# Kernel tuning notes

Hardware: AMD Instinct MI355X
Metric: run time of the kernel (lower is better)

## Reference

```python
import jax, jax.numpy as jnp
import numpy as np

D_MODEL = 1024
HEADS = 16
DEPTH = D_MODEL // HEADS
B, S = 2, 2048


def setup_inputs() -> dict:
    key = jax.random.key(0)
    ks = jax.random.split(key, 12)
    s = 1.0 / np.sqrt(D_MODEL)
    return {
        "q": jax.random.normal(ks[0], (B, S, D_MODEL), jnp.float32),
        "k": jax.random.normal(ks[1], (B, S, D_MODEL), jnp.float32),
        "v": jax.random.normal(ks[2], (B, S, D_MODEL), jnp.float32),
        "mask": jnp.zeros((B, 1, 1, S), jnp.float32),
        "wq": jax.random.normal(ks[3], (D_MODEL, D_MODEL), jnp.float32) * s,
        "bq": jnp.zeros((D_MODEL,), jnp.float32),
        "wk": jax.random.normal(ks[4], (D_MODEL, D_MODEL), jnp.float32) * s,
        "bk": jnp.zeros((D_MODEL,), jnp.float32),
        "wv": jax.random.normal(ks[5], (D_MODEL, D_MODEL), jnp.float32) * s,
        "bv": jnp.zeros((D_MODEL,), jnp.float32),
        "wo": jax.random.normal(ks[6], (D_MODEL, D_MODEL), jnp.float32) * s,
        "bo": jnp.zeros((D_MODEL,), jnp.float32),
    }


def _split_heads(x):
    b, s, _ = x.shape
    return x.reshape(b, s, HEADS, DEPTH).transpose(0, 2, 1, 3)  # [B,H,S,D]


def reference(q, k, v, mask, wq, bq, wk, bk, wv, bv, wo, bo):
    qh = _split_heads(q @ wq + bq)
    kh = _split_heads(k @ wk + bk)
    vh = _split_heads(v @ wv + bv)
    scale = 1.0 / jnp.sqrt(jnp.asarray(DEPTH, jnp.float32))
    scores = jnp.einsum("bhqd,bhkd->bhqk", qh, kh) * scale
    scores = scores + mask * -1e9
    attn = jax.nn.softmax(scores, axis=-1)  # [B,H,Sq,Sk]
    ctx = jnp.einsum("bhqk,bhkd->bhqd", attn, vh)
    ctx = ctx.transpose(0, 2, 1, 3).reshape(q.shape[0], -1, D_MODEL)
    out = ctx @ wo + bo
    return out, attn
```

## Files before the change

kernel.cpp:

```cpp
#include <hip/hip_runtime.h>
#include <cstdint>
#include <cstddef>

#define DEV __device__ __forceinline__

typedef __attribute__((ext_vector_type(8))) __bf16 bf16x8;
typedef __attribute__((ext_vector_type(4))) float f32x4;
typedef __attribute__((ext_vector_type(4))) uint32_t u32x4;

constexpr int BB = 2, SS = 2048, DMOD = 1024, HH = 16, DDEP = 64;
constexpr int MM = BB * SS;
constexpr float SCL = 0.125f;

constexpr size_t SZ_ACT = (size_t)MM * DMOD * 2;
constexpr size_t SZ_W = (size_t)DMOD * DMOD * 2;
constexpr size_t OFF_QB = 0;
constexpr size_t OFF_KB = OFF_QB + SZ_ACT;
constexpr size_t OFF_VB = OFF_KB + SZ_ACT;
constexpr size_t OFF_WQT = OFF_VB + SZ_ACT;
constexpr size_t OFF_WKT = OFF_WQT + SZ_W;
constexpr size_t OFF_WVT = OFF_WKT + SZ_W;
constexpr size_t OFF_WOT = OFF_WVT + SZ_W;
constexpr size_t OFF_QH = OFF_WOT + SZ_W;
constexpr size_t OFF_KH = OFF_QH + SZ_ACT;
constexpr size_t OFF_VH = OFF_KH + SZ_ACT;
constexpr size_t OFF_VHT = OFF_QB;
constexpr size_t OFF_CTX = OFF_KB;

DEV uint16_t f2bf(float f) {
  uint32_t u = __builtin_bit_cast(uint32_t, f);
  u += 0x7fffu + ((u >> 16) & 1u);
  return (uint16_t)(u >> 16);
}
DEV uint32_t pk2(float a, float b) { return (uint32_t)f2bf(a) | ((uint32_t)f2bf(b) << 16); }
DEV f32x4 mfma16(bf16x8 a, bf16x8 b, f32x4 c) {
  return __builtin_amdgcn_mfma_f32_16x16x32_bf16(a, b, c, 0, 0, 0);
}

__global__ __launch_bounds__(256) void cast_bf16(const float4* __restrict__ in, u32x4* __restrict__ out) {
  size_t i = (size_t)blockIdx.x * 256 + threadIdx.x;
  float4 a = in[i * 2], b = in[i * 2 + 1];
  u32x4 o;
  o.x = pk2(a.x, a.y); o.y = pk2(a.z, a.w);
  o.z = pk2(b.x, b.y); o.w = pk2(b.z, b.w);
  out[i] = o;
}

__global__ __launch_bounds__(256) void wtrans(const float* __restrict__ W, uint16_t* __restrict__ WT) {
  __shared__ uint16_t tile[64 * 72];
  const int kb = blockIdx.x * 64, nb = blockIdx.y * 64;
  const int t = threadIdx.x;
  {
    const int kl = t >> 2, nc = (t & 3) * 16;
    const float4* src = reinterpret_cast<const float4*>(&W[(size_t)(kb + kl) * DMOD + nb + nc]);
    float4 v0 = src[0], v1 = src[1], v2 = src[2], v3 = src[3];
    uint16_t* d = &tile[kl * 72 + nc];
    d[0] = f2bf(v0.x); d[1] = f2bf(v0.y); d[2] = f2bf(v0.z); d[3] = f2bf(v0.w);
    d[4] = f2bf(v1.x); d[5] = f2bf(v1.y); d[6] = f2bf(v1.z); d[7] = f2bf(v1.w);
    d[8] = f2bf(v2.x); d[9] = f2bf(v2.y); d[10] = f2bf(v2.z); d[11] = f2bf(v2.w);
    d[12] = f2bf(v3.x); d[13] = f2bf(v3.y); d[14] = f2bf(v3.z); d[15] = f2bf(v3.w);
  }
  __syncthreads();
  {
    const int n = t >> 2, kc = (t & 3) * 16;
    uint16_t r[16];
#pragma unroll
    for (int j = 0; j < 16; ++j) r[j] = tile[(kc + j) * 72 + n];
    u32x4 o0, o1;
    o0.x = r[0] | ((uint32_t)r[1] << 16);  o0.y = r[2] | ((uint32_t)r[3] << 16);
    o0.z = r[4] | ((uint32_t)r[5] << 16);  o0.w = r[6] | ((uint32_t)r[7] << 16);
    o1.x = r[8] | ((uint32_t)r[9] << 16);  o1.y = r[10] | ((uint32_t)r[11] << 16);
    o1.z = r[12] | ((uint32_t)r[13] << 16); o1.w = r[14] | ((uint32_t)r[15] << 16);
    uint16_t* dst = &WT[(size_t)(nb + n) * DMOD + kb + kc];
    *reinterpret_cast<u32x4*>(dst) = o0;
    *reinterpret_cast<u32x4*>(dst + 8) = o1;
  }
}

__global__ __launch_bounds__(256) void vtrans(const uint16_t* __restrict__ Vh, uint16_t* __restrict__ VhT) {
  __shared__ uint16_t tile[64 * 72];
  const int sb = blockIdx.x * 64;
  const int bh = blockIdx.y;
  const int b = bh >> 4, h = bh & 15;
  const int t = threadIdx.x;
  {
    const int sl = t >> 2, dc = (t & 3) * 16;
    const u32x4* src = reinterpret_cast<const u32x4*>(&Vh[(size_t)(b * SS + sb + sl) * DMOD + h * DDEP + dc]);
    *reinterpret_cast<u32x4*>(&tile[sl * 72 + dc]) = src[0];
    *reinterpret_cast<u32x4*>(&tile[sl * 72 + dc + 8]) = src[1];
  }
  __syncthreads();
  {
    const int d = t >> 2, sc = (t & 3) * 16;
    uint16_t r[16];
#pragma unroll
    for (int j = 0; j < 16; ++j) r[j] = tile[(sc + j) * 72 + d];
    u32x4 o0, o1;
    o0.x = r[0] | ((uint32_t)r[1] << 16);  o0.y = r[2] | ((uint32_t)r[3] << 16);
    o0.z = r[4] | ((uint32_t)r[5] << 16);  o0.w = r[6] | ((uint32_t)r[7] << 16);
    o1.x = r[8] | ((uint32_t)r[9] << 16);  o1.y = r[10] | ((uint32_t)r[11] << 16);
    o1.z = r[12] | ((uint32_t)r[13] << 16); o1.w = r[14] | ((uint32_t)r[15] << 16);
    uint16_t* dst = &VhT[((size_t)bh * DDEP + d) * SS + sb + sc];
    *reinterpret_cast<u32x4*>(dst) = o0;
    *reinterpret_cast<u32x4*>(dst + 8) = o1;
  }
}

template <int OUTF32>
__global__ __launch_bounds__(256) void gemm_bt(
    const uint16_t* __restrict__ A, const uint16_t* __restrict__ Bt,
    const float* __restrict__ bias, void* __restrict__ Cout,
    int Md, int Nd, int Kd) {
  __shared__ uint16_t As[128 * 64];
  __shared__ uint16_t Bs[128 * 64];
  const int t = threadIdx.x;
  const int lane = t & 63, w = t >> 6;
  const int wr = w >> 1, wc = w & 1;
  const int g = lane >> 4, r16 = lane & 15;
  const int ntiles = Nd >> 7;
  const int mt = blockIdx.x / ntiles, nt = blockIdx.x % ntiles;
  char* AsB = reinterpret_cast<char*>(As);
  char* BsB = reinterpret_cast<char*>(Bs);

  f32x4 acc[4][4] = {};
  const int nkt = Kd >> 6;
  for (int kt = 0; kt < nkt; ++kt) {
#pragma unroll
    for (int i = 0; i < 4; ++i) {
      int idx = i * 256 + t;
      int row = idx >> 3, ch = idx & 7;
      int sw = row * 128 + ((ch * 16) ^ ((row & 7) << 4));
      *reinterpret_cast<u32x4*>(AsB + sw) =
          *reinterpret_cast<const u32x4*>(A + (size_t)(mt * 128 + row) * Kd + kt * 64 + ch * 8);
      *reinterpret_cast<u32x4*>(BsB + sw) =
          *reinterpret_cast<const u32x4*>(Bt + (size_t)(nt * 128 + row) * Kd + kt * 64 + ch * 8);
    }
    __syncthreads();
#pragma unroll
    for (int kk = 0; kk < 2; ++kk) {
      bf16x8 af[4], bfr[4];
#pragma unroll
      for (int mf = 0; mf < 4; ++mf) {
        int row = wr * 64 + mf * 16 + r16;
        af[mf] = *reinterpret_cast<const bf16x8*>(AsB + row * 128 + ((kk * 64 + g * 16) ^ ((row & 7) << 4)));
      }
#pragma unroll
      for (int nf = 0; nf < 4; ++nf) {
        int row = wc * 64 + nf * 16 + r16;
        bfr[nf] = *reinterpret_cast<const bf16x8*>(BsB + row * 128 + ((kk * 64 + g * 16) ^ ((row & 7) << 4)));
      }
#pragma unroll
      for (int mf = 0; mf < 4; ++mf)
#pragma unroll
        for (int nf = 0; nf < 4; ++nf)
          acc[mf][nf] = mfma16(af[mf], bfr[nf], acc[mf][nf]);
    }
    __syncthreads();
  }
  float bv[4];
#pragma unroll
  for (int nf = 0; nf < 4; ++nf) bv[nf] = bias[nt * 128 + wc * 64 + nf * 16 + r16];
#pragma unroll
  for (int mf = 0; mf < 4; ++mf)
#pragma unroll
    for (int nf = 0; nf < 4; ++nf)
#pragma unroll
      for (int r = 0; r < 4; ++r) {
        int row = mt * 128 + wr * 64 + mf * 16 + g * 4 + r;
        int col = nt * 128 + wc * 64 + nf * 16 + r16;
        float v0 = acc[mf][nf][r] + bv[nf];
        if (OUTF32)
          reinterpret_cast<float*>(Cout)[(size_t)row * Nd + col] = v0;
        else
          reinterpret_cast<uint16_t*>(Cout)[(size_t)row * Nd + col] = f2bf(v0);
      }
}

__global__ __launch_bounds__(256) void attn_fused(
    const uint16_t* __restrict__ Qh, const uint16_t* __restrict__ Kh,
    const uint16_t* __restrict__ VhT, const float* __restrict__ mask,
    float* __restrict__ attn, uint16_t* __restrict__ ctx) {
  __shared__ uint16_t Plds[4 * 32 * 128];
  const int t = threadIdx.x;
  const int lane = t & 63, w = t >> 6;
  const int g = lane >> 4, c16 = lane & 15;
  const int bid = blockIdx.x;
  const int bh = bid >> 4, qt = bid & 15;
  const int b = bh >> 4, h = bh & 15;

  const uint16_t* Qbase = Qh + ((size_t)(b * SS + qt * 128 + w * 32)) * DMOD + h * DDEP;
  const uint16_t* Kbase = Kh + ((size_t)b * SS) * DMOD + h * DDEP;
  const uint16_t* Vbase = VhT + (size_t)bh * DDEP * SS;
  const float* mbase = mask + (size_t)b * SS;
  char* Pw = reinterpret_cast<char*>(Plds) + w * (32 * 256);

  bf16x8 qf[2][2];
#pragma unroll
  for (int rf = 0; rf < 2; ++rf)
#pragma unroll
    for (int kk = 0; kk < 2; ++kk)
      qf[rf][kk] = *reinterpret_cast<const bf16x8*>(Qbase + (size_t)(rf * 16 + c16) * DMOD + kk * 32 + g * 8);

  float m_[2][4], l_[2][4];
#pragma unroll
  for (int rf = 0; rf < 2; ++rf)
#pragma unroll
    for (int r = 0; r < 4; ++r) { m_[rf][r] = -3.0e38f; l_[rf][r] = 0.f; }

  for (int kt = 0; kt < 16; ++kt) {
    f32x4 sacc[2][8] = {};
#pragma unroll
    for (int nf = 0; nf < 8; ++nf) {
      const uint16_t* kp = Kbase + (size_t)(kt * 128 + nf * 16 + c16) * DMOD + g * 8;
      bf16x8 b0 = *reinterpret_cast<const bf16x8*>(kp);
      bf16x8 b1 = *reinterpret_cast<const bf16x8*>(kp + 32);
      sacc[0][nf] = mfma16(qf[0][0], b0, sacc[0][nf]);
      sacc[0][nf] = mfma16(qf[0][1], b1, sacc[0][nf]);
      sacc[1][nf] = mfma16(qf[1][0], b0, sacc[1][nf]);
      sacc[1][nf] = mfma16(qf[1][1], b1, sacc[1][nf]);
    }
    float mv[8];
#pragma unroll
    for (int nf = 0; nf < 8; ++nf) mv[nf] = mbase[kt * 128 + nf * 16 + c16] * -1e9f;
#pragma unroll
    for (int rf = 0; rf < 2; ++rf) {
#pragma unroll
      for (int r = 0; r < 4; ++r) {
        float tm = -3.0e38f;
#pragma unroll
        for (int nf = 0; nf < 8; ++nf) {
          float sv = sacc[rf][nf][r] * SCL + mv[nf];
          sacc[rf][nf][r] = sv;
          tm = fmaxf(tm, sv);
        }
#pragma unroll
        for (int d = 1; d < 16; d <<= 1) tm = fmaxf(tm, __shfl_xor(tm, d));
        float mo = m_[rf][r];
        float mn = fmaxf(mo, tm);
        float sum = 0.f;
#pragma unroll
        for (int nf = 0; nf < 8; ++nf) sum += __expf(sacc[rf][nf][r] - mn);
#pragma unroll
        for (int d = 1; d < 16; d <<= 1) sum += __shfl_xor(sum, d);
        l_[rf][r] = l_[rf][r] * __expf(mo - mn) + sum;
        m_[rf][r] = mn;
      }
    }
  }
  float li[2][4];
#pragma unroll
  for (int rf = 0; rf < 2; ++rf)
#pragma unroll
    for (int r = 0; r < 4; ++r) li[rf][r] = 1.f / l_[rf][r];

  f32x4 cacc[2][4] = {};
  float* abase = attn + ((size_t)bh * SS + qt * 128 + w * 32) * SS;

  for (int kt = 0; kt < 16; ++kt) {
    f32x4 sacc[2][8] = {};
#pragma unroll
    for (int nf = 0; nf < 8; ++nf) {
      const uint16_t* kp = Kbase + (size_t)(kt * 128 + nf * 16 + c16) * DMOD + g * 8;
      bf16x8 b0 = *reinterpret_cast<const bf16x8*>(kp);
      bf16x8 b1 = *reinterpret_cast<const bf16x8*>(kp + 32);
      sacc[0][nf] = mfma16(qf[0][0], b0, sacc[0][nf]);
      sacc[0][nf] = mfma16(qf[0][1], b1, sacc[0][nf]);
      sacc[1][nf] = mfma16(qf[1][0], b0, sacc[1][nf]);
      sacc[1][nf] = mfma16(qf[1][1], b1, sacc[1][nf]);
    }
    float mv[8];
#pragma unroll
    for (int nf = 0; nf < 8; ++nf) mv[nf] = mbase[kt * 128 + nf * 16 + c16] * -1e9f;
#pragma unroll
    for (int rf = 0; rf < 2; ++rf)
#pragma unroll
      for (int nf = 0; nf < 8; ++nf)
#pragma unroll
        for (int r = 0; r < 4; ++r) {
          int prow = rf * 16 + g * 4 + r;
          float p = __expf(sacc[rf][nf][r] * SCL + mv[nf] - m_[rf][r]) * li[rf][r];
          abase[(size_t)prow * SS + kt * 128 + nf * 16 + c16] = p;
          *reinterpret_cast<uint16_t*>(
              Pw + prow * 256 + (((nf * 16 + c16) * 2) ^ ((prow & 7) << 4))) = f2bf(p);
        }
#pragma unroll
    for (int kk = 0; kk < 4; ++kk) {
      bf16x8 pa[2];
#pragma unroll
      for (int rf = 0; rf < 2; ++rf) {
        int arow = rf * 16 + c16;
        pa[rf] = *reinterpret_cast<const bf16x8*>(
            Pw + arow * 256 + ((kk * 64 + g * 16) ^ ((arow & 7) << 4)));
      }
#pragma unroll
      for (int nf = 0; nf < 4; ++nf) {
        bf16x8 vf = *reinterpret_cast<const bf16x8*>(
            Vbase + (size_t)(nf * 16 + c16) * SS + kt * 128 + kk * 32 + g * 8);
        cacc[0][nf] = mfma16(pa[0], vf, cacc[0][nf]);
        cacc[1][nf] = mfma16(pa[1], vf, cacc[1][nf]);
      }
    }
  }
#pragma unroll
  for (int rf = 0; rf < 2; ++rf)
#pragma unroll
    for (int nf = 0; nf < 4; ++nf)
#pragma unroll
      for (int r = 0; r < 4; ++r) {
        int row = qt * 128 + w * 32 + rf * 16 + g * 4 + r;
        ctx[((size_t)(b * SS + row)) * DMOD + h * DDEP + nf * 16 + c16] = f2bf(cacc[rf][nf][r]);
      }
}

extern "C" void kernel_launch(void* const* d_in, const int* in_sizes, int n_in,
                              void* d_out, int out_size, void* d_ws, size_t ws_size,
                              hipStream_t stream) {
  (void)in_sizes; (void)n_in; (void)out_size; (void)ws_size;
  const float* q = (const float*)d_in[0];
  const float* k = (const float*)d_in[1];
  const float* v = (const float*)d_in[2];
  const float* mask = (const float*)d_in[3];
  const float* wq = (const float*)d_in[4];
  const float* bq = (const float*)d_in[5];
  const float* wk = (const float*)d_in[6];
  const float* bk = (const float*)d_in[7];
  const float* wv = (const float*)d_in[8];
  const float* bvv = (const float*)d_in[9];
  const float* wo = (const float*)d_in[10];
  const float* bo = (const float*)d_in[11];

  char* ws = (char*)d_ws;
  uint16_t* qb = (uint16_t*)(ws + OFF_QB);
  uint16_t* kb = (uint16_t*)(ws + OFF_KB);
  uint16_t* vb = (uint16_t*)(ws + OFF_VB);
  uint16_t* wqT = (uint16_t*)(ws + OFF_WQT);
  uint16_t* wkT = (uint16_t*)(ws + OFF_WKT);
  uint16_t* wvT = (uint16_t*)(ws + OFF_WVT);
  uint16_t* woT = (uint16_t*)(ws + OFF_WOT);
  uint16_t* Qhp = (uint16_t*)(ws + OFF_QH);
  uint16_t* Khp = (uint16_t*)(ws + OFF_KH);
  uint16_t* Vhp = (uint16_t*)(ws + OFF_VH);
  uint16_t* VhTp = (uint16_t*)(ws + OFF_VHT);
  uint16_t* ctxp = (uint16_t*)(ws + OFF_CTX);

  float* outp = (float*)d_out;
  float* attnp = outp + (size_t)MM * DMOD;

  cast_bf16<<<2048, 256, 0, stream>>>((const float4*)q, (u32x4*)qb);
  cast_bf16<<<2048, 256, 0, stream>>>((const float4*)k, (u32x4*)kb);
  cast_bf16<<<2048, 256, 0, stream>>>((const float4*)v, (u32x4*)vb);
  wtrans<<<dim3(16, 16), 256, 0, stream>>>(wq, wqT);
  wtrans<<<dim3(16, 16), 256, 0, stream>>>(wk, wkT);
  wtrans<<<dim3(16, 16), 256, 0, stream>>>(wv, wvT);
  wtrans<<<dim3(16, 16), 256, 0, stream>>>(wo, woT);
  gemm_bt<0><<<256, 256, 0, stream>>>(qb, wqT, bq, Qhp, MM, DMOD, DMOD);
  gemm_bt<0><<<256, 256, 0, stream>>>(kb, wkT, bk, Khp, MM, DMOD, DMOD);
  gemm_bt<0><<<256, 256, 0, stream>>>(vb, wvT, bvv, Vhp, MM, DMOD, DMOD);
  vtrans<<<dim3(32, 32), 256, 0, stream>>>(Vhp, VhTp);
  attn_fused<<<512, 256, 0, stream>>>(Qhp, Khp, VhTp, mask, attnp, ctxp);
  gemm_bt<1><<<256, 256, 0, stream>>>(ctxp, woT, bo, d_out, MM, DMOD, DMOD);
}
```

Measured before the change: 952.7 us.

## Coalesce attention-prob stores via LDS staging, shrink tiles, use direct global-to-LDS loads

The attention kernel now stages fp32 probabilities in swizzled LDS and writes the attn matrix with coalesced float4 rows instead of scattered scalar stores. It also reuses that buffer for the bf16 P operand of the PV matmul. GEMM and attention tiles are halved (64x64 and 16 rows per wave) so each launch has 1024 blocks, with a block-index remap for locality and occupancy hints. GEMM tiles are loaded through global_load_lds. The attn write traffic dominates, so coalescing it is the main target. The cost is less operand reuse per block and more K/V reloads.

```diff
diff --git a/kernel.cpp b/kernel.cpp
--- a/kernel.cpp
+++ b/kernel.cpp
@@ -36,6 +36,12 @@
 DEV f32x4 mfma16(bf16x8 a, bf16x8 b, f32x4 c) {
   return __builtin_amdgcn_mfma_f32_16x16x32_bf16(a, b, c, 0, 0, 0);
 }
+DEV void gload16(const void* g, void* l) {
+  __builtin_amdgcn_global_load_lds(
+      (const __attribute__((address_space(1))) void*)g,
+      (__attribute__((address_space(3))) void*)l, 16, 0, 0);
+}
+DEV int pswz(int row) { return ((row & 7) << 5) ^ ((row & 8) << 1); }
 
 __global__ __launch_bounds__(256) void cast_bf16(const float4* __restrict__ in, u32x4* __restrict__ out) {
   size_t i = (size_t)blockIdx.x * 256 + threadIdx.x;
@@ -107,67 +113,74 @@
 }
 
 template <int OUTF32>
-__global__ __launch_bounds__(256) void gemm_bt(
+__global__ __launch_bounds__(256, 4) void gemm_bt(
     const uint16_t* __restrict__ A, const uint16_t* __restrict__ Bt,
     const float* __restrict__ bias, void* __restrict__ Cout,
     int Md, int Nd, int Kd) {
-  __shared__ uint16_t As[128 * 64];
-  __shared__ uint16_t Bs[128 * 64];
+  __shared__ uint16_t As[64 * 64];
+  __shared__ uint16_t Bs[64 * 64];
   const int t = threadIdx.x;
   const int lane = t & 63, w = t >> 6;
   const int wr = w >> 1, wc = w & 1;
-  const int g = lane >> 4, r16 = lane & 15;
-  const int ntiles = Nd >> 7;
-  const int mt = blockIdx.x / ntiles, nt = blockIdx.x % ntiles;
+  const int g = lane >> 4, c16 = lane & 15;
+  const int ntiles = Nd >> 6;
+  const int nwg = (Md >> 6) * ntiles;
+  int bid = blockIdx.x;
+  bid = (bid & 7) * (nwg >> 3) + (bid >> 3);
+  const int mt = bid / ntiles, nt = bid % ntiles;
   char* AsB = reinterpret_cast<char*>(As);
   char* BsB = reinterpret_cast<char*>(Bs);
 
-  f32x4 acc[4][4] = {};
+  const int srow = w * 8 + (lane >> 3);
+  const int schunk0 = lane & 7;
+
+  f32x4 acc[2][2] = {};
   const int nkt = Kd >> 6;
   for (int kt = 0; kt < nkt; ++kt) {
 #pragma unroll
-    for (int i = 0; i < 4; ++i) {
-      int idx = i * 256 + t;
-      int row = idx >> 3, ch = idx & 7;
-      int sw = row * 128 + ((ch * 16) ^ ((row & 7) << 4));
-      *reinterpret_cast<u32x4*>(AsB + sw) =
-          *reinterpret_cast<const u32x4*>(A + (size_t)(mt * 128 + row) * Kd + kt * 64 + ch * 8);
-      *reinterpret_cast<u32x4*>(BsB + sw) =
-          *reinterpret_cast<const u32x4*>(Bt + (size_t)(nt * 128 + row) * Kd + kt * 64 + ch * 8);
+    for (int i = 0; i < 2; ++i) {
+      int row = i * 32 + srow;
+      int cs = schunk0 ^ (row & 7);
+      gload16(A + (size_t)(mt * 64 + row) * Kd + kt * 64 + cs * 8,
+              AsB + i * 4096 + w * 1024);
+      gload16(Bt + (size_t)(nt * 64 + row) * Kd + kt * 64 + cs * 8,
+              BsB + i * 4096 + w * 1024);
     }
     __syncthreads();
 #pragma unroll
     for (int kk = 0; kk < 2; ++kk) {
-      bf16x8 af[4], bfr[4];
-#pragma unroll
-      for (int mf = 0; mf < 4; ++mf) {
-        int row = wr * 64 + mf * 16 + r16;
-        af[mf] = *reinterpret_cast<const bf16x8*>(AsB + row * 128 + ((kk * 64 + g * 16) ^ ((row & 7) << 4)));
-      }
-#pragma unroll
-      for (int nf = 0; nf < 4; ++nf) {
-        int row = wc * 64 + nf * 16 + r16;
-        bfr[nf] = *reinterpret_cast<const bf16x8*>(BsB + row * 128 + ((kk * 64 + g * 16) ^ ((row & 7) << 4)));
-      }
-#pragma unroll
-      for (int mf = 0; mf < 4; ++mf)
-#pragma unroll
-        for (int nf = 0; nf < 4; ++nf)
+      bf16x8 af[2], bfr[2];
+#pragma unroll
+      for (int mf = 0; mf < 2; ++mf) {
+        int row = wr * 32 + mf * 16 + c16;
+        af[mf] = *reinterpret_cast<const bf16x8*>(
+            AsB + row * 128 + ((kk * 4 + g) ^ (row & 7)) * 16);
+      }
+#pragma unroll
+      for (int nf = 0; nf < 2; ++nf) {
+        int row = wc * 32 + nf * 16 + c16;
+        bfr[nf] = *reinterpret_cast<const bf16x8*>(
+            BsB + row * 128 + ((kk * 4 + g) ^ (row & 7)) * 16);
+      }
+#pragma unroll
+      for (int mf = 0; mf < 2; ++mf)
+#pragma unroll
+        for (int nf = 0; nf < 2; ++nf)
           acc[mf][nf] = mfma16(af[mf], bfr[nf], acc[mf][nf]);
     }
     __syncthreads();
   }
-  float bv[4];
-#pragma unroll
-  for (int nf = 0; nf < 4; ++nf) bv[nf] = bias[nt * 128 + wc * 64 + nf * 16 + r16];
-#pragma unroll
-  for (int mf = 0; mf < 4; ++mf)
-#pragma unroll
-    for (int nf = 0; nf < 4; ++nf)
+  float bv[2];
+#pragma unroll
+  for (int nf = 0; nf < 2; ++nf) bv[nf] = bias[nt * 64 + wc * 32 + nf * 16 + c16];
+#pragma unroll
+  for (int mf = 0; mf < 2; ++mf)
+#pragma unroll
+    for (int nf = 0; nf < 2; ++nf)
 #pragma unroll
       for (int r = 0; r < 4; ++r) {
-        int row = mt * 128 + wr * 64 + mf * 16 + g * 4 + r;
-        int col = nt * 128 + wc * 64 + nf * 16 + r16;
+        int row = mt * 64 + wr * 32 + mf * 16 + g * 4 + r;
+        int col = nt * 64 + wc * 32 + nf * 16 + c16;
         float v0 = acc[mf][nf][r] + bv[nf];
         if (OUTF32)
           reinterpret_cast<float*>(Cout)[(size_t)row * Nd + col] = v0;
@@ -176,140 +189,129 @@
       }
 }
 
-__global__ __launch_bounds__(256) void attn_fused(
+__global__ __launch_bounds__(256, 4) void attn_fused(
     const uint16_t* __restrict__ Qh, const uint16_t* __restrict__ Kh,
     const uint16_t* __restrict__ VhT, const float* __restrict__ mask,
     float* __restrict__ attn, uint16_t* __restrict__ ctx) {
-  __shared__ uint16_t Plds[4 * 32 * 128];
+  __shared__ float Plds[4 * 16 * 128];
   const int t = threadIdx.x;
   const int lane = t & 63, w = t >> 6;
   const int g = lane >> 4, c16 = lane & 15;
-  const int bid = blockIdx.x;
-  const int bh = bid >> 4, qt = bid & 15;
+  int bid = blockIdx.x;
+  bid = (bid & 7) * 128 + (bid >> 3);
+  const int bh = bid >> 5, qt = bid & 31;
   const int b = bh >> 4, h = bh & 15;
 
-  const uint16_t* Qbase = Qh + ((size_t)(b * SS + qt * 128 + w * 32)) * DMOD + h * DDEP;
+  const uint16_t* Qbase = Qh + ((size_t)(b * SS + qt * 64 + w * 16)) * DMOD + h * DDEP;
   const uint16_t* Kbase = Kh + ((size_t)b * SS) * DMOD + h * DDEP;
   const uint16_t* Vbase = VhT + (size_t)bh * DDEP * SS;
   const float* mbase = mask + (size_t)b * SS;
-  char* Pw = reinterpret_cast<char*>(Plds) + w * (32 * 256);
-
-  bf16x8 qf[2][2];
-#pragma unroll
-  for (int rf = 0; rf < 2; ++rf)
-#pragma unroll
-    for (int kk = 0; kk < 2; ++kk)
-      qf[rf][kk] = *reinterpret_cast<const bf16x8*>(Qbase + (size_t)(rf * 16 + c16) * DMOD + kk * 32 + g * 8);
-
-  float m_[2][4], l_[2][4];
-#pragma unroll
-  for (int rf = 0; rf < 2; ++rf)
-#pragma unroll
-    for (int r = 0; r < 4; ++r) { m_[rf][r] = -3.0e38f; l_[rf][r] = 0.f; }
+  char* Pw = reinterpret_cast<char*>(Plds) + w * (16 * 512);
+
+  bf16x8 qf[2];
+#pragma unroll
+  for (int kk = 0; kk < 2; ++kk)
+    qf[kk] = *reinterpret_cast<const bf16x8*>(Qbase + (size_t)c16 * DMOD + kk * 32 + g * 8);
+
+  float m_[4], l_[4];
+#pragma unroll
+  for (int r = 0; r < 4; ++r) { m_[r] = -3.0e38f; l_[r] = 0.f; }
 
   for (int kt = 0; kt < 16; ++kt) {
-    f32x4 sacc[2][8] = {};
+    f32x4 sacc[8] = {};
 #pragma unroll
     for (int nf = 0; nf < 8; ++nf) {
       const uint16_t* kp = Kbase + (size_t)(kt * 128 + nf * 16 + c16) * DMOD + g * 8;
       bf16x8 b0 = *reinterpret_cast<const bf16x8*>(kp);
       bf16x8 b1 = *reinterpret_cast<const bf16x8*>(kp + 32);
-      sacc[0][nf] = mfma16(qf[0][0], b0, sacc[0][nf]);
-      sacc[0][nf] = mfma16(qf[0][1], b1, sacc[0][nf]);
-      sacc[1][nf] = mfma16(qf[1][0], b0, sacc[1][nf]);
-      sacc[1][nf] = mfma16(qf[1][1], b1, sacc[1][nf]);
+      sacc[nf] = mfma16(qf[0], b0, sacc[nf]);
+      sacc[nf] = mfma16(qf[1], b1, sacc[nf]);
     }
     float mv[8];
 #pragma unroll
     for (int nf = 0; nf < 8; ++nf) mv[nf] = mbase[kt * 128 + nf * 16 + c16] * -1e9f;
 #pragma unroll
-    for (int rf = 0; rf < 2; ++rf) {
-#pragma unroll
-      for (int r = 0; r < 4; ++r) {
-        float tm = -3.0e38f;
-#pragma unroll
-        for (int nf = 0; nf < 8; ++nf) {
-          float sv = sacc[rf][nf][r] * SCL + mv[nf];
-          sacc[rf][nf][r] = sv;
-          tm = fmaxf(tm, sv);
-        }
-#pragma unroll
-        for (int d = 1; d < 16; d <<= 1) tm = fmaxf(tm, __shfl_xor(tm, d));
-        float mo = m_[rf][r];
-        float mn = fmaxf(mo, tm);
-        float sum = 0.f;
-#pragma unroll
-        for (int nf = 0; nf < 8; ++nf) sum += __expf(sacc[rf][nf][r] - mn);
-#pragma unroll
-        for (int d = 1; d < 16; d <<= 1) sum += __shfl_xor(sum, d);
-        l_[rf][r] = l_[rf][r] * __expf(mo - mn) + sum;
-        m_[rf][r] = mn;
-      }
-    }
-  }
-  float li[2][4];
-#pragma unroll
-  for (int rf = 0; rf < 2; ++rf)
-#pragma unroll
-    for (int r = 0; r < 4; ++r) li[rf][r] = 1.f / l_[rf][r];
-
-  f32x4 cacc[2][4] = {};
-  float* abase = attn + ((size_t)bh * SS + qt * 128 + w * 32) * SS;
+    for (int r = 0; r < 4; ++r) {
+      float tm = -3.0e38f;
+#pragma unroll
+      for (int nf = 0; nf < 8; ++nf) {
+        float sv = sacc[nf][r] * SCL + mv[nf];
+        sacc[nf][r] = sv;
+        tm = fmaxf(tm, sv);
+      }
+#pragma unroll
+      for (int d = 1; d < 16; d <<= 1) tm = fmaxf(tm, __shfl_xor(tm, d));
+      float mo = m_[r];
+      float mn = fmaxf(mo, tm);
+      float sum = 0.f;
+#pragma unroll
+      for (int nf = 0; nf < 8; ++nf) sum += __expf(sacc[nf][r] - mn);
+#pragma unroll
+      for (int d = 1; d < 16; d <<= 1) sum += __shfl_xor(sum, d);
+      l_[r] = l_[r] * __expf(mo - mn) + sum;
+      m_[r] = mn;
+    }
+  }
+  float li[4];
+#pragma unroll
+  for (int r = 0; r < 4; ++r) li[r] = 1.f / l_[r];
+
+  f32x4 cacc[4] = {};
+  float* abase = attn + ((size_t)bh * SS + qt * 64 + w * 16) * SS;
 
   for (int kt = 0; kt < 16; ++kt) {
-    f32x4 sacc[2][8] = {};
+    f32x4 sacc[8] = {};
 #pragma unroll
     for (int nf = 0; nf < 8; ++nf) {
       const uint16_t* kp = Kbase + (size_t)(kt * 128 + nf * 16 + c16) * DMOD + g * 8;
       bf16x8 b0 = *reinterpret_cast<const bf16x8*>(kp);
       bf16x8 b1 = *reinterpret_cast<const bf16x8*>(kp + 32);
-      sacc[0][nf] = mfma16(qf[0][0], b0, sacc[0][nf]);
-      sacc[0][nf] = mfma16(qf[0][1], b1, sacc[0][nf]);
-      sacc[1][nf] = mfma16(qf[1][0], b0, sacc[1][nf]);
-      sacc[1][nf] = mfma16(qf[1][1], b1, sacc[1][nf]);
+      sacc[nf] = mfma16(qf[0], b0, sacc[nf]);
+      sacc[nf] = mfma16(qf[1], b1, sacc[nf]);
     }
     float mv[8];
 #pragma unroll
     for (int nf = 0; nf < 8; ++nf) mv[nf] = mbase[kt * 128 + nf * 16 + c16] * -1e9f;
 #pragma unroll
-    for (int rf = 0; rf < 2; ++rf)
-#pragma unroll
-      for (int nf = 0; nf < 8; ++nf)
-#pragma unroll
-        for (int r = 0; r < 4; ++r) {
-          int prow = rf * 16 + g * 4 + r;
-          float p = __expf(sacc[rf][nf][r] * SCL + mv[nf] - m_[rf][r]) * li[rf][r];
-          abase[(size_t)prow * SS + kt * 128 + nf * 16 + c16] = p;
-          *reinterpret_cast<uint16_t*>(
-              Pw + prow * 256 + (((nf * 16 + c16) * 2) ^ ((prow & 7) << 4))) = f2bf(p);
-        }
-#pragma unroll
-    for (int kk = 0; kk < 4; ++kk) {
-      bf16x8 pa[2];
-#pragma unroll
-      for (int rf = 0; rf < 2; ++rf) {
-        int arow = rf * 16 + c16;
-        pa[rf] = *reinterpret_cast<const bf16x8*>(
-            Pw + arow * 256 + ((kk * 64 + g * 16) ^ ((arow & 7) << 4)));
-      }
+    for (int nf = 0; nf < 8; ++nf)
+#pragma unroll
+      for (int r = 0; r < 4; ++r) {
+        int pr = g * 4 + r;
+        float p = __expf(sacc[nf][r] * SCL + mv[nf] - m_[r]) * li[r];
+        *reinterpret_cast<float*>(
+            Pw + pr * 512 + (((nf * 16 + c16) * 4) ^ pswz(pr))) = p;
+      }
+#pragma unroll
+    for (int i = 0; i < 8; ++i) {
+      int row = i * 2 + (lane >> 5);
+      int cc = lane & 31;
+      float4 val = *reinterpret_cast<const float4*>(
+          Pw + row * 512 + ((cc * 16) ^ pswz(row)));
+      *reinterpret_cast<float4*>(abase + (size_t)row * SS + kt * 128 + cc * 4) = val;
+    }
+#pragma unroll
+    for (int ks = 0; ks < 4; ++ks) {
+      const char* prow = Pw + c16 * 512;
+      f32x4 p0 = *reinterpret_cast<const f32x4*>(prow + ((ks * 128 + g * 32) ^ pswz(c16)));
+      f32x4 p1 = *reinterpret_cast<const f32x4*>(prow + ((ks * 128 + g * 32 + 16) ^ pswz(c16)));
+      union { bf16x8 v; uint16_t u[8]; } pa;
+#pragma unroll
+      for (int j = 0; j < 4; ++j) { pa.u[j] = f2bf(p0[j]); pa.u[4 + j] = f2bf(p1[j]); }
 #pragma unroll
       for (int nf = 0; nf < 4; ++nf) {
         bf16x8 vf = *reinterpret_cast<const bf16x8*>(
-            Vbase + (size_t)(nf * 16 + c16) * SS + kt * 128 + kk * 32 + g * 8);
-        cacc[0][nf] = mfma16(pa[0], vf, cacc[0][nf]);
-        cacc[1][nf] = mfma16(pa[1], vf, cacc[1][nf]);
-      }
-    }
-  }
-#pragma unroll
-  for (int rf = 0; rf < 2; ++rf)
-#pragma unroll
-    for (int nf = 0; nf < 4; ++nf)
-#pragma unroll
-      for (int r = 0; r < 4; ++r) {
-        int row = qt * 128 + w * 32 + rf * 16 + g * 4 + r;
-        ctx[((size_t)(b * SS + row)) * DMOD + h * DDEP + nf * 16 + c16] = f2bf(cacc[rf][nf][r]);
-      }
+            Vbase + (size_t)(nf * 16 + c16) * SS + kt * 128 + ks * 32 + g * 8);
+        cacc[nf] = mfma16(pa.v, vf, cacc[nf]);
+      }
+    }
+  }
+#pragma unroll
+  for (int nf = 0; nf < 4; ++nf)
+#pragma unroll
+    for (int r = 0; r < 4; ++r) {
+      int row = qt * 64 + w * 16 + g * 4 + r;
+      ctx[((size_t)(b * SS + row)) * DMOD + h * DDEP + nf * 16 + c16] = f2bf(cacc[nf][r]);
+    }
 }
 
 extern "C" void kernel_launch(void* const* d_in, const int* in_sizes, int n_in,
@@ -353,10 +355,10 @@
   wtrans<<<dim3(16, 16), 256, 0, stream>>>(wk, wkT);
   wtrans<<<dim3(16, 16), 256, 0, stream>>>(wv, wvT);
   wtrans<<<dim3(16, 16), 256, 0, stream>>>(wo, woT);
-  gemm_bt<0><<<256, 256, 0, stream>>>(qb, wqT, bq, Qhp, MM, DMOD, DMOD);
-  gemm_bt<0><<<256, 256, 0, stream>>>(kb, wkT, bk, Khp, MM, DMOD, DMOD);
-  gemm_bt<0><<<256, 256, 0, stream>>>(vb, wvT, bvv, Vhp, MM, DMOD, DMOD);
+  gemm_bt<0><<<1024, 256, 0, stream>>>(qb, wqT, bq, Qhp, MM, DMOD, DMOD);
+  gemm_bt<0><<<1024, 256, 0, stream>>>(kb, wkT, bk, Khp, MM, DMOD, DMOD);
+  gemm_bt<0><<<1024, 256, 0, stream>>>(vb, wvT, bvv, Vhp, MM, DMOD, DMOD);
   vtrans<<<dim3(32, 32), 256, 0, stream>>>(Vhp, VhTp);
-  attn_fused<<<512, 256, 0, stream>>>(Qhp, Khp, VhTp, mask, attnp, ctxp);
-  gemm_bt<1><<<256, 256, 0, stream>>>(ctxp, woT, bo, d_out, MM, DMOD, DMOD);
-}
+  attn_fused<<<1024, 256, 0, stream>>>(Qhp, Khp, VhTp, mask, attnp, ctxp);
+  gemm_bt<1><<<1024, 256, 0, stream>>>(ctxp, woT, bo, d_out, MM, DMOD, DMOD);
+}
```

Result: slower. 1.006 ms (+5.6%).
